# Kernel tuning notes

Hardware: AMD Instinct MI355X
Metric: run time of the kernel (lower is better)

The kernel has to match this reference:

```python
import jax, jax.numpy as jnp
import numpy as np

N_NODES = 50000
N_EDGES = 800000
D_FEAT = 64      # node feature dim -> edge input is 2*D_FEAT
HIDDEN = 128     # ebm hidden width (== 2*D_FEAT here)


def setup_inputs() -> dict:
    key = jax.random.key(0)
    ks = jax.random.split(key, 8)
    x = jax.random.normal(ks[0], (N_NODES, D_FEAT), dtype=jnp.float32)
    edge_index = jax.random.randint(ks[1], (2, N_EDGES), 0, N_NODES, dtype=jnp.int64)
    t = jax.random.uniform(ks[2], (N_EDGES,), dtype=jnp.float32)
    s1 = 1.0 / np.sqrt(2 * D_FEAT)
    s2 = 1.0 / np.sqrt(HIDDEN)
    W1 = jax.random.normal(ks[3], (2 * D_FEAT, HIDDEN), dtype=jnp.float32) * s1
    b1 = jnp.zeros((HIDDEN,), dtype=jnp.float32)
    Wt = jax.random.normal(ks[4], (1, HIDDEN), dtype=jnp.float32)
    bt = jnp.zeros((HIDDEN,), dtype=jnp.float32)
    W2 = jax.random.normal(ks[5], (HIDDEN, 2 * D_FEAT), dtype=jnp.float32) * s2
    b2 = jnp.zeros((2 * D_FEAT,), dtype=jnp.float32)
    return {"x": x, "edge_index": edge_index, "t": t,
            "W1": W1, "b1": b1, "Wt": Wt, "bt": bt, "W2": W2, "b2": b2}


def _ebm(edge_input, t, W1, b1, Wt, bt, W2, b2):
    # time-conditioned 2-layer SiLU MLP: [E, 2d] -> [E, 2d]
    t_emb = jax.nn.silu(t[:, None] * Wt + bt)            # [E, H]
    h = jax.nn.silu(edge_input @ W1 + t_emb + b1)        # [E, H]
    return h @ W2 + b2                                    # [E, 2d]


def reference(x, edge_index, t, W1, b1, Wt, bt, W2, b2):
    row, col = edge_index[0], edge_index[1]
    # gather endpoint features and concat -> [E, 2d]
    edge_input = jnp.concatenate([x[row], x[col]], axis=1)
    edge_output = _ebm(edge_input, t, W1, b1, Wt, bt, W2, b2)
    d = edge_output.shape[1] // 2
    src_update = edge_output[:, :d]
    tgt_update = edge_output[:, d:]
    update = jnp.concatenate([src_update, tgt_update], axis=0)  # [2E, d]
    idx = jnp.concatenate([row, col], axis=0)                   # [2E]
    # scatter_add into node slots
    return jax.ops.segment_sum(update, idx, num_segments=x.shape[0])
```

## Files before the change

kernel.cpp:

```cpp
#include <hip/hip_runtime.h>
#include <hip/hip_bf16.h>

#define NEDGE 800000
#define NNODE 50000
#define DF    64
#define HID   128
#define NTILE (NEDGE / 16)

using short8 = __attribute__((ext_vector_type(8))) short;
using f32x4  = __attribute__((ext_vector_type(4))) float;
using i32x4  = __attribute__((ext_vector_type(4))) int;

union P8 { unsigned int u[4]; short8 s; };

__device__ __forceinline__ unsigned int pk2(float lo, float hi) {
    union { __hip_bfloat162 p; unsigned int u; } c;
    c.p = __float22bfloat162_rn(float2{lo, hi});
    return c.u;
}

__device__ __forceinline__ short8 cvt8(f32x4 u, f32x4 v) {
    P8 p;
    p.u[0] = pk2(u[0], u[1]);
    p.u[1] = pk2(u[2], u[3]);
    p.u[2] = pk2(v[0], v[1]);
    p.u[3] = pk2(v[2], v[3]);
    return p.s;
}

__device__ __forceinline__ unsigned short bf1(float f) {
    union { __hip_bfloat16 b; unsigned short u; } c;
    c.b = __float2bfloat16(f);
    return c.u;
}

__device__ __forceinline__ float bf2f(unsigned short u) {
    union { unsigned int i; float f; } c;
    c.i = ((unsigned int)u) << 16;
    return c.f;
}

__device__ __forceinline__ float exp2_hw(float x) {
    float r; asm("v_exp_f32 %0, %1" : "=v"(r) : "v"(x)); return r;
}
__device__ __forceinline__ float rcp_hw(float x) {
    float r; asm("v_rcp_f32 %0, %1" : "=v"(r) : "v"(x)); return r;
}
__device__ __forceinline__ float silu_f(float v) {
    return v * rcp_hw(1.0f + exp2_hw(v * -1.44269504f));
}

__device__ __forceinline__ int swz(int r, int k) {
    return (r << 8) + ((((k >> 3) ^ (r & 7)) << 4) | ((k & 7) << 1));
}
__device__ __forceinline__ int swz16(int r, int slot) {
    return (r << 8) + ((slot ^ (r & 7)) << 4);
}

__global__ void __launch_bounds__(256) hist_kernel(const int* __restrict__ ei,
                                                   int* __restrict__ counts) {
    const int i = blockIdx.x * 256 + threadIdx.x;
    if (i < 2 * NEDGE) atomicAdd(&counts[ei[i]], 1);
}

__global__ void __launch_bounds__(1024) scan1_kernel(const int* __restrict__ counts,
                                                     int* __restrict__ offs,
                                                     int* __restrict__ bsum) {
    __shared__ int buf[1024];
    const int tid = threadIdx.x;
    const int gid = blockIdx.x * 1024 + tid;
    const int v = (gid < NNODE) ? counts[gid] : 0;
    buf[tid] = v;
    __syncthreads();
#pragma unroll
    for (int off = 1; off < 1024; off <<= 1) {
        const int u = (tid >= off) ? buf[tid - off] : 0;
        __syncthreads();
        buf[tid] += u;
        __syncthreads();
    }
    if (gid < NNODE) offs[gid] = buf[tid] - v;
    if (tid == 1023) bsum[blockIdx.x] = buf[1023];
}

__global__ void __launch_bounds__(1024) scan2_kernel(int* __restrict__ bsum, int nb) {
    __shared__ int buf[1024];
    const int tid = threadIdx.x;
    const int v = (tid < nb) ? bsum[tid] : 0;
    buf[tid] = v;
    __syncthreads();
#pragma unroll
    for (int off = 1; off < 1024; off <<= 1) {
        const int u = (tid >= off) ? buf[tid - off] : 0;
        __syncthreads();
        buf[tid] += u;
        __syncthreads();
    }
    if (tid < nb) bsum[tid] = buf[tid] - v;
}

__global__ void __launch_bounds__(1024) scan3_kernel(int* __restrict__ offs,
                                                     const int* __restrict__ bsum,
                                                     int* __restrict__ cursor) {
    const int gid = blockIdx.x * 1024 + threadIdx.x;
    if (gid < NNODE) {
        const int o = offs[gid] + bsum[blockIdx.x];
        offs[gid] = o;
        cursor[gid] = o;
    }
    if (gid == 0) offs[NNODE] = 2 * NEDGE;
}

__global__ void __launch_bounds__(256, 2)
gnn_mlp_scatter(const float* __restrict__ x, const int* __restrict__ ei,
                const float* __restrict__ t,
                const float* __restrict__ W1, const float* __restrict__ b1,
                const float* __restrict__ Wt, const float* __restrict__ bt,
                const float* __restrict__ W2, const float* __restrict__ b2,
                unsigned short* __restrict__ eout, int* __restrict__ cursor)
{
    extern __shared__ char lds[];
    char* const w1s = lds;
    char* const w2s = lds + 32768;
    const int tid  = threadIdx.x;
    const int wave = tid >> 6;
    const int lane = tid & 63;
    char* const hs = lds + 65536 + (wave << 12);

    for (int idx = tid; idx < HID * HID; idx += 256) {
        const int k = idx >> 7, j = idx & 127;
        *(unsigned short*)(w1s + swz(j, k)) = bf1(W1[idx]);
        const int rho = ((j & 7) << 4) + (j >> 3);
        *(unsigned short*)(w2s + swz(rho, k)) = bf1(W2[idx]);
    }

    const int jl   = lane & 15;
    const int quad = lane >> 4;
    const int k0   = quad << 3;
    float wtj[8], btj[8], b1j[8], b2j[8];
#pragma unroll
    for (int nt = 0; nt < 8; nt++) {
        const int j = nt * 16 + jl;
        wtj[nt] = Wt[j]; btj[nt] = bt[j]; b1j[nt] = b1[j];
        b2j[nt] = b2[jl * 8 + nt];
    }
    __syncthreads();

    const int gwave = (blockIdx.x << 2) + wave;
    const int nwave = gridDim.x << 2;

#define ISSUE_EI(T, RA, CA) { const int e_ = (T) * 16 + jl; RA = ei[e_]; CA = ei[NEDGE + e_]; }
#define ISSUE_X(RA, CA, X_) { \
    const float* xr_ = x + (RA) * DF + k0; \
    const float* xc_ = x + (CA) * DF + k0; \
    X_[0] = *(const f32x4*)(xr_);      X_[1] = *(const f32x4*)(xr_ + 4);  \
    X_[2] = *(const f32x4*)(xr_ + 32); X_[3] = *(const f32x4*)(xr_ + 36); \
    X_[4] = *(const f32x4*)(xc_);      X_[5] = *(const f32x4*)(xc_ + 4);  \
    X_[6] = *(const f32x4*)(xc_ + 32); X_[7] = *(const f32x4*)(xc_ + 36); }
#define ISSUE_EP(T, T4_, RI_, CI_) { const int er_ = (T) * 16 + (quad << 2); \
    T4_ = *(const f32x4*)(t + er_); \
    RI_ = *(const i32x4*)(ei + er_); \
    CI_ = *(const i32x4*)(ei + NEDGE + er_); }

    int tile = gwave;
    if (tile < NTILE) {
        int riA, ciA;  ISSUE_EI(tile, riA, ciA);
        f32x4 X[8];    ISSUE_X(riA, ciA, X);
        f32x4 T4; i32x4 RI, CI; ISSUE_EP(tile, T4, RI, CI);
        int tn  = tile + nwave;
        int tns = (tn < NTILE) ? tn : gwave;
        int riA_n, ciA_n; ISSUE_EI(tns, riA_n, ciA_n);

        while (tile < NTILE) {
            f32x4 Xn[8]; ISSUE_X(riA_n, ciA_n, Xn);
            f32x4 T4n; i32x4 RIn, CIn; ISSUE_EP(tns, T4n, RIn, CIn);
            const int t2  = tn + nwave;
            const int t2s = (t2 < NTILE) ? t2 : gwave;
            int riA_nn, ciA_nn; ISSUE_EI(t2s, riA_nn, ciA_nn);

            int posS[4], posT[4];
            {
                unsigned int ps[4], pt[4];
#pragma unroll
                for (int r = 0; r < 4; r++) {
                    ps[r] = (jl == 0) ? atomicAdd((unsigned int*)&cursor[RI[r]], 1u) : 0u;
                    pt[r] = (jl == 8) ? atomicAdd((unsigned int*)&cursor[CI[r]], 1u) : 0u;
                }
#pragma unroll
                for (int r = 0; r < 4; r++) {
                    posS[r] = __shfl((int)ps[r], lane & 48);
                    posT[r] = __shfl((int)pt[r], (lane & 48) | 8);
                }
            }

            short8 a[4];
#pragma unroll
            for (int kk = 0; kk < 4; kk++) a[kk] = cvt8(X[2 * kk], X[2 * kk + 1]);

#pragma unroll
            for (int nt = 0; nt < 8; nt++) {
                f32x4 acc = {0.f, 0.f, 0.f, 0.f};
                const int j = nt * 16 + jl;
#pragma unroll
                for (int kk = 0; kk < 4; kk++) {
                    const short8 bfr = *(const short8*)(w1s + swz16(j, (kk << 2) + quad));
                    acc = __builtin_amdgcn_mfma_f32_16x16x32_bf16(a[kk], bfr, acc, 0, 0, 0);
                }
#pragma unroll
                for (int r = 0; r < 4; r++) {
                    const float temb = silu_f(fmaf(T4[r], wtj[nt], btj[nt]));
                    const float h = silu_f(acc[r] + temb + b1j[nt]);
                    *(unsigned short*)(hs + swz((quad << 2) + r, j)) = bf1(h);
                }
            }

            short8 a2[4];
#pragma unroll
            for (int kk = 0; kk < 4; kk++) {
                a2[kk] = *(const short8*)(hs + swz16(jl, (kk << 2) + quad));
            }

            f32x4 acc2[8];
#pragma unroll
            for (int nt = 0; nt < 8; nt++) {
                f32x4 acc = {0.f, 0.f, 0.f, 0.f};
                const int rho = nt * 16 + jl;
#pragma unroll
                for (int kk = 0; kk < 4; kk++) {
                    const short8 bfr = *(const short8*)(w2s + swz16(rho, (kk << 2) + quad));
                    acc = __builtin_amdgcn_mfma_f32_16x16x32_bf16(a2[kk], bfr, acc, 0, 0, 0);
                }
                acc2[nt] = acc;
            }

#pragma unroll
            for (int r = 0; r < 4; r++) {
                const int pos = (jl < 8) ? posS[r] : posT[r];
                unsigned short* dst = eout + (size_t)pos * 64 + ((jl & 7) << 3);
                P8 p;
                p.u[0] = pk2(acc2[0][r] + b2j[0], acc2[1][r] + b2j[1]);
                p.u[1] = pk2(acc2[2][r] + b2j[2], acc2[3][r] + b2j[3]);
                p.u[2] = pk2(acc2[4][r] + b2j[4], acc2[5][r] + b2j[5]);
                p.u[3] = pk2(acc2[6][r] + b2j[6], acc2[7][r] + b2j[7]);
                *(short8*)dst = p.s;
            }

            tile = tn; tn = t2; tns = t2s;
#pragma unroll
            for (int i = 0; i < 8; i++) X[i] = Xn[i];
            T4 = T4n; RI = RIn; CI = CIn;
            riA_n = riA_nn; ciA_n = ciA_nn;
        }
    }
#undef ISSUE_EI
#undef ISSUE_X
#undef ISSUE_EP
}

__global__ void __launch_bounds__(256)
gather_kernel(const unsigned short* __restrict__ eout, const int* __restrict__ offs,
              float* __restrict__ out)
{
    const int wave = threadIdx.x >> 6;
    const int lane = threadIdx.x & 63;
    const int n = blockIdx.x * 4 + wave;
    if (n >= NNODE) return;
    const int o0 = offs[n], o1 = offs[n + 1];

    const int cg = lane & 7;
    const int rp = lane >> 3;
    float acc[8] = {0.f, 0.f, 0.f, 0.f, 0.f, 0.f, 0.f, 0.f};
    for (int k = o0 + rp; k < o1; k += 8) {
        const short8 v = *(const short8*)(eout + (size_t)k * 64 + (cg << 3));
#pragma unroll
        for (int j = 0; j < 8; j++) acc[j] += bf2f((unsigned short)v[j]);
    }
#pragma unroll
    for (int j = 0; j < 8; j++) {
        acc[j] += __shfl_xor(acc[j], 8);
        acc[j] += __shfl_xor(acc[j], 16);
        acc[j] += __shfl_xor(acc[j], 32);
    }
    if (rp == 0) {
        float* o = out + (size_t)n * DF + (cg << 3);
        *(f32x4*)(o)     = f32x4{acc[0], acc[1], acc[2], acc[3]};
        *(f32x4*)(o + 4) = f32x4{acc[4], acc[5], acc[6], acc[7]};
    }
}

__global__ void __launch_bounds__(256, 2)
gnn_fused_atomic(const float* __restrict__ x, const int* __restrict__ ei,
                 const float* __restrict__ t,
                 const float* __restrict__ W1, const float* __restrict__ b1,
                 const float* __restrict__ Wt, const float* __restrict__ bt,
                 const float* __restrict__ W2, const float* __restrict__ b2,
                 float* __restrict__ out)
{
    extern __shared__ char lds[];
    char* const w1s = lds;
    char* const w2s = lds + 32768;
    const int tid  = threadIdx.x;
    const int wave = tid >> 6;
    const int lane = tid & 63;
    char* const hs = lds + 65536 + (wave << 12);

    for (int idx = tid; idx < HID * HID; idx += 256) {
        const int k = idx >> 7, j = idx & 127;
        const int off = swz(j, k);
        *(unsigned short*)(w1s + off) = bf1(W1[idx]);
        *(unsigned short*)(w2s + off) = bf1(W2[idx]);
    }

    const int jl   = lane & 15;
    const int quad = lane >> 4;
    const int k0   = quad << 3;
    float wtj[8], btj[8], b1j[8], b2j[8];
#pragma unroll
    for (int nt = 0; nt < 8; nt++) {
        const int j = nt * 16 + jl;
        wtj[nt] = Wt[j]; btj[nt] = bt[j]; b1j[nt] = b1[j]; b2j[nt] = b2[j];
    }
    __syncthreads();

    const int gwave = (blockIdx.x << 2) + wave;
    const int nwave = gridDim.x << 2;

    for (int tile = gwave; tile < NTILE; tile += nwave) {
        const int base = tile << 4;
        const int eA = base + jl;
        const int ri = ei[eA];
        const int ci = ei[NEDGE + eA];

        short8 a[4];
        {
            const float* xr_ = x + ri * DF + k0;
            const float* xc_ = x + ci * DF + k0;
            a[0] = cvt8(*(const f32x4*)(xr_),      *(const f32x4*)(xr_ + 4));
            a[1] = cvt8(*(const f32x4*)(xr_ + 32), *(const f32x4*)(xr_ + 36));
            a[2] = cvt8(*(const f32x4*)(xc_),      *(const f32x4*)(xc_ + 4));
            a[3] = cvt8(*(const f32x4*)(xc_ + 32), *(const f32x4*)(xc_ + 36));
        }

        const int er = base + (quad << 2);
        const f32x4 T4 = *(const f32x4*)(t + er);
        const i32x4 RI = *(const i32x4*)(ei + er);
        const i32x4 CI = *(const i32x4*)(ei + NEDGE + er);

#pragma unroll
        for (int nt = 0; nt < 8; nt++) {
            f32x4 acc = {0.f, 0.f, 0.f, 0.f};
            const int j = nt * 16 + jl;
#pragma unroll
            for (int kk = 0; kk < 4; kk++) {
                const short8 bfr = *(const short8*)(w1s + swz16(j, (kk << 2) + quad));
                acc = __builtin_amdgcn_mfma_f32_16x16x32_bf16(a[kk], bfr, acc, 0, 0, 0);
            }
#pragma unroll
            for (int r = 0; r < 4; r++) {
                const float temb = silu_f(fmaf(T4[r], wtj[nt], btj[nt]));
                const float h = silu_f(acc[r] + temb + b1j[nt]);
                *(unsigned short*)(hs + swz((quad << 2) + r, j)) = bf1(h);
            }
        }

        short8 a2[4];
#pragma unroll
        for (int kk = 0; kk < 4; kk++) {
            a2[kk] = *(const short8*)(hs + swz16(jl, (kk << 2) + quad));
        }

#pragma unroll
        for (int nt = 0; nt < 8; nt++) {
            f32x4 acc = {0.f, 0.f, 0.f, 0.f};
            const int j = nt * 16 + jl;
#pragma unroll
            for (int kk = 0; kk < 4; kk++) {
                const short8 bfr = *(const short8*)(w2s + swz16(j, (kk << 2) + quad));
                acc = __builtin_amdgcn_mfma_f32_16x16x32_bf16(a2[kk], bfr, acc, 0, 0, 0);
            }
#pragma unroll
            for (int r = 0; r < 4; r++) {
                const float v = acc[r] + b2j[nt];
                const int node = (nt < 4) ? RI[r] : CI[r];
                unsafeAtomicAdd(out + node * DF + (j & 63), v);
            }
        }
    }
}

extern "C" void kernel_launch(void* const* d_in, const int* in_sizes, int n_in,
                              void* d_out, int out_size, void* d_ws, size_t ws_size,
                              hipStream_t stream) {
    const float* x  = (const float*)d_in[0];
    const int*   ei = (const int*)d_in[1];
    const float* t  = (const float*)d_in[2];
    const float* W1 = (const float*)d_in[3];
    const float* b1 = (const float*)d_in[4];
    const float* Wt = (const float*)d_in[5];
    const float* bt = (const float*)d_in[6];
    const float* W2 = (const float*)d_in[7];
    const float* b2 = (const float*)d_in[8];
    float* out = (float*)d_out;

    const int ldsBytes = 65536 + 4 * 4096;

    const size_t eoutB = (size_t)(2 * NEDGE) * 64 * sizeof(unsigned short);
    const size_t need  = eoutB + (size_t)(3 * NNODE + 1 + 1024) * sizeof(int) + 256;

    if (ws_size >= need) {
        char* wsb = (char*)d_ws;
        unsigned short* eout = (unsigned short*)wsb;
        int* counts = (int*)(wsb + eoutB);
        int* offs   = counts + NNODE;
        int* bsum   = offs + NNODE + 1;
        int* cursor = bsum + 1024;

        const int nsb = (NNODE + 1023) / 1024;

        (void)hipMemsetAsync(counts, 0, (size_t)NNODE * sizeof(int), stream);
        hipLaunchKernelGGL(hist_kernel, dim3((2 * NEDGE + 255) / 256), dim3(256), 0, stream,
                           ei, counts);
        hipLaunchKernelGGL(scan1_kernel, dim3(nsb), dim3(1024), 0, stream,
                           counts, offs, bsum);
        hipLaunchKernelGGL(scan2_kernel, dim3(1), dim3(1024), 0, stream, bsum, nsb);
        hipLaunchKernelGGL(scan3_kernel, dim3(nsb), dim3(1024), 0, stream,
                           offs, bsum, cursor);

        (void)hipFuncSetAttribute((const void*)gnn_mlp_scatter,
                                  hipFuncAttributeMaxDynamicSharedMemorySize, ldsBytes);
        hipLaunchKernelGGL(gnn_mlp_scatter, dim3(512), dim3(256), ldsBytes, stream,
                           x, ei, t, W1, b1, Wt, bt, W2, b2, eout, cursor);

        hipLaunchKernelGGL(gather_kernel, dim3((NNODE + 3) / 4), dim3(256), 0, stream,
                           eout, offs, out);
    } else {
        (void)hipMemsetAsync(out, 0, (size_t)out_size * sizeof(float), stream);
        (void)hipFuncSetAttribute((const void*)gnn_fused_atomic,
                                  hipFuncAttributeMaxDynamicSharedMemorySize, ldsBytes);
        hipLaunchKernelGGL(gnn_fused_atomic, dim3(512), dim3(256), ldsBytes, stream,
                           x, ei, t, W1, b1, Wt, bt, W2, b2, out);
    }
}
```

Baseline: 256.7 us.

## Use 12-wave blocks sharing LDS weights and vectorize hidden-layer LDS stores

The MLP-scatter kernel now runs 768-thread blocks (12 waves) that share a single LDS copy of W1/W2, instead of 256-thread blocks. This cuts per-wave LDS weight duplication and the weight-staging cost per wave, and the grid drops to 256 blocks. W1 columns are permuted the same way as W2, so each lane owns 8 contiguous hidden units and can write them to LDS as one packed 16-byte bf16 store instead of eight 2-byte stores. The risks are higher register pressure from holding all eight accumulators at once, and a scheduling change from launch_bounds(768,3).

```diff
diff --git a/kernel.cpp b/kernel.cpp
--- a/kernel.cpp
+++ b/kernel.cpp
@@ -6,6 +6,8 @@
 #define DF    64
 #define HID   128
 #define NTILE (NEDGE / 16)
+#define BLK   768
+#define WPB   12
 
 using short8 = __attribute__((ext_vector_type(8))) short;
 using f32x4  = __attribute__((ext_vector_type(4))) float;
@@ -111,7 +113,7 @@
     if (gid == 0) offs[NNODE] = 2 * NEDGE;
 }
 
-__global__ void __launch_bounds__(256, 2)
+__global__ void __launch_bounds__(BLK, 3)
 gnn_mlp_scatter(const float* __restrict__ x, const int* __restrict__ ei,
                 const float* __restrict__ t,
                 const float* __restrict__ W1, const float* __restrict__ b1,
@@ -127,10 +129,10 @@
     const int lane = tid & 63;
     char* const hs = lds + 65536 + (wave << 12);
 
-    for (int idx = tid; idx < HID * HID; idx += 256) {
+    for (int idx = tid; idx < HID * HID; idx += BLK) {
         const int k = idx >> 7, j = idx & 127;
-        *(unsigned short*)(w1s + swz(j, k)) = bf1(W1[idx]);
         const int rho = ((j & 7) << 4) + (j >> 3);
+        *(unsigned short*)(w1s + swz(rho, k)) = bf1(W1[idx]);
         *(unsigned short*)(w2s + swz(rho, k)) = bf1(W2[idx]);
     }
 
@@ -140,14 +142,13 @@
     float wtj[8], btj[8], b1j[8], b2j[8];
 #pragma unroll
     for (int nt = 0; nt < 8; nt++) {
-        const int j = nt * 16 + jl;
-        wtj[nt] = Wt[j]; btj[nt] = bt[j]; b1j[nt] = b1[j];
-        b2j[nt] = b2[jl * 8 + nt];
+        const int j = jl * 8 + nt;
+        wtj[nt] = Wt[j]; btj[nt] = bt[j]; b1j[nt] = b1[j]; b2j[nt] = b2[j];
     }
     __syncthreads();
 
-    const int gwave = (blockIdx.x << 2) + wave;
-    const int nwave = gridDim.x << 2;
+    const int gwave = blockIdx.x * WPB + wave;
+    const int nwave = gridDim.x * WPB;
 
 #define ISSUE_EI(T, RA, CA) { const int e_ = (T) * 16 + jl; RA = ei[e_]; CA = ei[NEDGE + e_]; }
 #define ISSUE_X(RA, CA, X_) { \
@@ -197,21 +198,33 @@
 #pragma unroll
             for (int kk = 0; kk < 4; kk++) a[kk] = cvt8(X[2 * kk], X[2 * kk + 1]);
 
+            f32x4 acc1[8];
 #pragma unroll
             for (int nt = 0; nt < 8; nt++) {
                 f32x4 acc = {0.f, 0.f, 0.f, 0.f};
-                const int j = nt * 16 + jl;
+                const int rho = nt * 16 + jl;
 #pragma unroll
                 for (int kk = 0; kk < 4; kk++) {
-                    const short8 bfr = *(const short8*)(w1s + swz16(j, (kk << 2) + quad));
+                    const short8 bfr = *(const short8*)(w1s + swz16(rho, (kk << 2) + quad));
                     acc = __builtin_amdgcn_mfma_f32_16x16x32_bf16(a[kk], bfr, acc, 0, 0, 0);
                 }
-#pragma unroll
-                for (int r = 0; r < 4; r++) {
+                acc1[nt] = acc;
+            }
+
+#pragma unroll
+            for (int r = 0; r < 4; r++) {
+                float h[8];
+#pragma unroll
+                for (int nt = 0; nt < 8; nt++) {
                     const float temb = silu_f(fmaf(T4[r], wtj[nt], btj[nt]));
-                    const float h = silu_f(acc[r] + temb + b1j[nt]);
-                    *(unsigned short*)(hs + swz((quad << 2) + r, j)) = bf1(h);
+                    h[nt] = silu_f(acc1[nt][r] + temb + b1j[nt]);
                 }
+                P8 p;
+                p.u[0] = pk2(h[0], h[1]);
+                p.u[1] = pk2(h[2], h[3]);
+                p.u[2] = pk2(h[4], h[5]);
+                p.u[3] = pk2(h[6], h[7]);
+                *(short8*)(hs + swz16((quad << 2) + r, jl)) = p.s;
             }
 
             short8 a2[4];
@@ -402,8 +415,6 @@
     const float* b2 = (const float*)d_in[8];
     float* out = (float*)d_out;
 
-    const int ldsBytes = 65536 + 4 * 4096;
-
     const size_t eoutB = (size_t)(2 * NEDGE) * 64 * sizeof(unsigned short);
     const size_t need  = eoutB + (size_t)(3 * NNODE + 1 + 1024) * sizeof(int) + 256;
 
@@ -426,14 +437,16 @@
         hipLaunchKernelGGL(scan3_kernel, dim3(nsb), dim3(1024), 0, stream,
                            offs, bsum, cursor);
 
+        const int ldsMlp = 65536 + WPB * 4096;
         (void)hipFuncSetAttribute((const void*)gnn_mlp_scatter,
-                                  hipFuncAttributeMaxDynamicSharedMemorySize, ldsBytes);
-        hipLaunchKernelGGL(gnn_mlp_scatter, dim3(512), dim3(256), ldsBytes, stream,
+                                  hipFuncAttributeMaxDynamicSharedMemorySize, ldsMlp);
+        hipLaunchKernelGGL(gnn_mlp_scatter, dim3(256), dim3(BLK), ldsMlp, stream,
                            x, ei, t, W1, b1, Wt, bt, W2, b2, eout, cursor);
 
         hipLaunchKernelGGL(gather_kernel, dim3((NNODE + 3) / 4), dim3(256), 0, stream,
                            eout, offs, out);
     } else {
+        const int ldsBytes = 65536 + 4 * 4096;
         (void)hipMemsetAsync(out, 0, (size_t)out_size * sizeof(float), stream);
         (void)hipFuncSetAttribute((const void*)gnn_fused_atomic,
                                   hipFuncAttributeMaxDynamicSharedMemorySize, ldsBytes);
```

After: 260.7 us. About the same (+1.6%).
